# Kernel tuning notes

Measured on AMD Instinct MI355X. Metric: run time of the kernel, lower is better.

The kernel has to match this reference:

```python
import jax, jax.numpy as jnp
import numpy as np

N_NODES = 100000
N_EDGES = 1000000
F = 64
ALPHA = 0.1
BETA = 0.5


def setup_inputs() -> dict:
    key = jax.random.key(0)
    k1, k2, k3, k4, k5, k6 = jax.random.split(key, 6)
    features = jax.random.normal(k1, (N_NODES, F), dtype=jnp.float32)
    features0 = jax.random.normal(k2, (N_NODES, F), dtype=jnp.float32)
    edge_src = jax.random.randint(k3, (N_EDGES,), 0, N_NODES, dtype=jnp.int32)
    edge_dst = jax.random.randint(k4, (N_EDGES,), 0, N_NODES, dtype=jnp.int32)
    edge_vals = jax.random.uniform(k5, (N_EDGES,), dtype=jnp.float32)
    W = jax.random.normal(k6, (F, F), dtype=jnp.float32) * (1.0 / np.sqrt(F))
    return {"features": features, "features0": features0, "edge_src": edge_src,
            "edge_dst": edge_dst, "edge_vals": edge_vals, "W": W}


def reference(features, features0, edge_src, edge_dst, edge_vals, W):
    # hi = A @ features  (sparse propagation via edge-list segment sum)
    msgs = features[edge_src] * edge_vals[:, None]           # [E, F]
    hi = jax.ops.segment_sum(msgs, edge_dst, num_segments=N_NODES)  # [N, F]
    # variant=False branch of GCNII-style layer
    support = (1.0 - ALPHA) * hi + ALPHA * features0          # [N, F]
    r = support
    output = BETA * (support @ W) + (1.0 - BETA) * r          # [N, F]
    return jax.nn.relu(output)
```

## Files before the change

### kernel.cpp

```cpp
#include <hip/hip_runtime.h>

#define N_NODES 100000
#define N_EDGES 1000000
#define FDIM    64
#define TILES   6250
#define CAP     36

#define MM_BLOCKS  1024
#define EPB        2048
#define BIN_BLOCKS ((N_EDGES + EPB - 1) / EPB)

#define NPART 196
#define PCAP  9216

#define SCAN_BLOCKS 391

#define B_CNT   0u
#define B_GCUR  450560u
#define B_BKT   524288u
#define B_GBF   14924288u
#define B_NEED  27800000u

#define C_DEG    0u
#define C_OFFS   524288u
#define C_CURSOR 1048576u
#define C_BSUM   1572864u
#define C_BOFF   1703936u
#define C_BPACK  2097152u
#define C_GBF    6291456u

typedef short bf16x8 __attribute__((ext_vector_type(8)));
typedef float f32x4  __attribute__((ext_vector_type(4)));

__device__ __forceinline__ short f2bf(float f) {
    unsigned u = __float_as_uint(f);
    u += 0x7fff + ((u >> 16) & 1);
    return (short)(u >> 16);
}

__device__ __forceinline__ unsigned packrec(int s, float v) {
    unsigned q = (unsigned)__float2int_rn(v * 32768.0f);
    q = q > 32767u ? 32767u : q;
    return ((unsigned)s << 15) | q;
}

__global__ __launch_bounds__(256, 2) void k_fused(
        const float* __restrict__ feat, const float* __restrict__ f0,
        const float* __restrict__ W, unsigned short* __restrict__ gbf,
        float* __restrict__ out,
        const int* __restrict__ src, const int* __restrict__ dst,
        const float* __restrict__ val, int* __restrict__ cnt,
        unsigned* __restrict__ bkt, int* __restrict__ gcur, int binBlocks) {

    if ((int)blockIdx.x < binBlocks) {
        __shared__ int            hist[256];
        __shared__ int            excl[256];
        __shared__ int            curs[256];
        __shared__ int            gbas[256];
        __shared__ unsigned short slotpid[EPB];
        __shared__ uint2          rbuf[EPB];

        int t = threadIdx.x;
        hist[t] = 0;
        __syncthreads();

        int e0 = blockIdx.x * EPB + t * 8;
        unsigned recx[8]; int dd[8]; int pid[8]; bool vld[8];
        if (e0 + 8 <= N_EDGES) {
            int4   sa = *(const int4*)(src + e0);
            int4   sb = *(const int4*)(src + e0 + 4);
            int4   da = *(const int4*)(dst + e0);
            int4   db = *(const int4*)(dst + e0 + 4);
            float4 va = *(const float4*)(val + e0);
            float4 vb = *(const float4*)(val + e0 + 4);
            int   s8[8] = {sa.x, sa.y, sa.z, sa.w, sb.x, sb.y, sb.z, sb.w};
            int   d8[8] = {da.x, da.y, da.z, da.w, db.x, db.y, db.z, db.w};
            float v8[8] = {va.x, va.y, va.z, va.w, vb.x, vb.y, vb.z, vb.w};
#pragma unroll
            for (int j = 0; j < 8; ++j) {
                recx[j] = packrec(s8[j], v8[j]);
                dd[j]   = d8[j];
                pid[j]  = d8[j] >> 9;
                vld[j]  = true;
            }
        } else {
#pragma unroll
            for (int j = 0; j < 8; ++j) {
                vld[j] = (e0 + j) < N_EDGES;
                if (vld[j]) {
                    recx[j] = packrec(src[e0 + j], val[e0 + j]);
                    dd[j]   = dst[e0 + j];
                    pid[j]  = dd[j] >> 9;
                } else { recx[j] = 0; dd[j] = 0; pid[j] = 0; }
            }
        }
#pragma unroll
        for (int j = 0; j < 8; ++j)
            if (vld[j]) atomicAdd(&hist[pid[j]], 1);
        __syncthreads();

        int myv = hist[t];
        for (int off = 1; off < 256; off <<= 1) {
            int add = (t >= off) ? hist[t - off] : 0;
            __syncthreads();
            hist[t] += add;
            __syncthreads();
        }
        excl[t] = hist[t] - myv;
        curs[t] = excl[t];
        gbas[t] = (t < NPART && myv > 0) ? atomicAdd(&gcur[t], myv) : 0;
        __syncthreads();

#pragma unroll
        for (int j = 0; j < 8; ++j)
            if (vld[j]) {
                int pos = atomicAdd(&curs[pid[j]], 1);
                rbuf[pos]    = make_uint2(recx[j], (unsigned)dd[j]);
                slotpid[pos] = (unsigned short)pid[j];
            }
        __syncthreads();

        int total = hist[255];
        uint2* pbuf = (uint2*)bkt;
        for (int i = t; i < total; i += 256) {
            int p   = slotpid[i];
            int off = gbas[p] + (i - excl[p]);
            if (off < PCAP)
                pbuf[(size_t)p * PCAP + off] = rbuf[i];
        }
        return;
    }

    int lane = threadIdx.x & 63;
    int mmb  = blockIdx.x - binBlocks;
    int wid  = mmb * 4 + (threadIdx.x >> 6);
    int nw   = (gridDim.x - binBlocks) * 4;
    int n16  = lane & 15, q = lane >> 4;

    bf16x8 bf[2][4];
#pragma unroll
    for (int s = 0; s < 2; ++s)
#pragma unroll
        for (int t = 0; t < 4; ++t) {
            bf16x8 b;
#pragma unroll
            for (int j = 0; j < 8; ++j) {
                int k = 32 * s + 8 * q + j, n = 16 * t + n16;
                float m = 0.5f * W[k * FDIM + n] + (k == n ? 0.5f : 0.0f);
                b[j] = f2bf(m);
            }
            bf[s][t] = b;
        }

    for (int tid = wid; tid < 2 * TILES; tid += nw) {
        bool hpath = tid >= TILES;
        int  row0  = (hpath ? tid - TILES : tid) * 16;
        const float* x = (hpath ? f0 : feat) + (size_t)row0 * FDIM;

        bf16x8 af[2];
#pragma unroll
        for (int s = 0; s < 2; ++s) {
            const float* xp = x + (size_t)n16 * FDIM + 32 * s + 8 * q;
            float4 u0 = *(const float4*)xp;
            float4 u1 = *(const float4*)(xp + 4);
            bf16x8 a;
            a[0] = f2bf(u0.x); a[1] = f2bf(u0.y); a[2] = f2bf(u0.z); a[3] = f2bf(u0.w);
            a[4] = f2bf(u1.x); a[5] = f2bf(u1.y); a[6] = f2bf(u1.z); a[7] = f2bf(u1.w);
            af[s] = a;
        }

        f32x4 acc[4] = {{0,0,0,0},{0,0,0,0},{0,0,0,0},{0,0,0,0}};
#pragma unroll
        for (int s = 0; s < 2; ++s)
#pragma unroll
            for (int t = 0; t < 4; ++t)
                acc[t] = __builtin_amdgcn_mfma_f32_16x16x32_bf16(af[s], bf[s][t], acc[t], 0, 0, 0);

        if (!hpath) {
#pragma unroll
            for (int t = 0; t < 4; ++t)
#pragma unroll
                for (int r = 0; r < 4; ++r)
                    gbf[(size_t)(row0 + 4 * q + r) * FDIM + 16 * t + n16] =
                        (unsigned short)f2bf(acc[t][r]);
        } else {
#pragma unroll
            for (int t = 0; t < 4; ++t)
#pragma unroll
                for (int r = 0; r < 4; ++r)
                    out[(size_t)(row0 + 4 * q + r) * FDIM + 16 * t + n16] =
                        0.1f * acc[t][r];
        }
    }
}

__global__ __launch_bounds__(256) void k_p2(
        unsigned* __restrict__ bkt, int* __restrict__ cnt,
        const int* __restrict__ gcur) {
    __shared__ int      lcnt[512];
    __shared__ unsigned lbkt[512 * CAP];

    int p = blockIdx.x, t = threadIdx.x;
    int nE = gcur[p];
    if (nE > PCAP) nE = PCAP;

    for (int i = t; i < 512; i += 256) lcnt[i] = 0;
    __syncthreads();

    const uint2* pb = (const uint2*)bkt + (size_t)p * PCAP;
    for (int e = t; e < nE; e += 256) {
        uint2 r  = pb[e];
        int   ld = (int)r.y - (p << 9);
        int  pos = atomicAdd(&lcnt[ld], 1);
        if (pos < CAP) lbkt[ld * CAP + pos] = r.x;
    }
    __syncthreads();

    int nbase = p << 9;
    int nnode = N_NODES - nbase; if (nnode > 512) nnode = 512;
    unsigned* gb = bkt + (size_t)nbase * CAP;
    for (int i = t; i < nnode * CAP; i += 256) gb[i] = lbkt[i];
    for (int i = t; i < nnode;       i += 256) cnt[nbase + i] = lcnt[i];
}

__device__ __forceinline__ void gather_core(int node, int lane,
                                            const unsigned* base, int deg,
                                            const unsigned short* gbf,
                                            float* out) {
    int fl  = lane & 31;
    int sub = lane >> 5;

    float2 h = ((const float2*)(out + (size_t)node * FDIM))[fl];
    float accLo = 0.0f, accHi = 0.0f;

    for (int e0 = 0; e0 < deg; e0 += 16) {
        unsigned rsel[8];
        float    vsel[8];
#pragma unroll
        for (int j = 0; j < 8; ++j) {
            int i0 = e0 + 2 * j, i1 = i0 + 1;
            int c0 = i0 < deg ? i0 : deg - 1;
            int c1 = i1 < deg ? i1 : deg - 1;
            unsigned rA = base[c0];
            unsigned rB = base[c1];
            unsigned r  = sub ? rB : rA;
            bool ok = (sub ? i1 : i0) < deg;
            rsel[j] = r;
            vsel[j] = ok ? (float)(r & 0x7fffu) * (1.0f / 32768.0f) : 0.0f;
        }
        unsigned u[8];
#pragma unroll
        for (int j = 0; j < 8; ++j)
            u[j] = *(const unsigned*)(gbf + (size_t)(rsel[j] >> 15) * FDIM + 2 * fl);
#pragma unroll
        for (int j = 0; j < 8; ++j) {
            accLo = fmaf(vsel[j], __uint_as_float(u[j] << 16), accLo);
            accHi = fmaf(vsel[j], __uint_as_float(u[j] & 0xffff0000u), accHi);
        }
    }
    accLo += __shfl_xor(accLo, 32);
    accHi += __shfl_xor(accHi, 32);
    if (sub == 0) {
        float2 r2;
        r2.x = fmaxf(0.9f * accLo + h.x, 0.0f);
        r2.y = fmaxf(0.9f * accHi + h.y, 0.0f);
        ((float2*)(out + (size_t)node * FDIM))[fl] = r2;
    }
}

__global__ __launch_bounds__(256, 8) void k_gather_b(
        const int* __restrict__ cnt, const unsigned* __restrict__ bkt,
        const unsigned short* __restrict__ gbf, float* __restrict__ out) {
    int gid  = blockIdx.x * blockDim.x + threadIdx.x;
    int node = __builtin_amdgcn_readfirstlane(gid >> 6);
    int lane = threadIdx.x & 63;
    if (node >= N_NODES) return;
    int c = cnt[node];
    int deg = __builtin_amdgcn_readfirstlane(c < CAP ? c : CAP);
    gather_core(node, lane, bkt + (size_t)node * CAP, deg, gbf, out);
}

__global__ __launch_bounds__(256, 8) void k_gather_c(
        const int* __restrict__ offs, const unsigned* __restrict__ bpack,
        const unsigned short* __restrict__ gbf, float* __restrict__ out) {
    int gid  = blockIdx.x * blockDim.x + threadIdx.x;
    int node = __builtin_amdgcn_readfirstlane(gid >> 6);
    int lane = threadIdx.x & 63;
    if (node >= N_NODES) return;
    int beg = __builtin_amdgcn_readfirstlane(offs[node]);
    int end = __builtin_amdgcn_readfirstlane(
        (node == N_NODES - 1) ? N_EDGES : offs[node + 1]);
    gather_core(node, lane, bpack + beg, end - beg, gbf, out);
}

__global__ void k_hist(const int* __restrict__ dst, int* __restrict__ deg) {
    int e = blockIdx.x * blockDim.x + threadIdx.x;
    if (e < N_EDGES) atomicAdd(&deg[dst[e]], 1);
}

__global__ void k_scan1(const int* __restrict__ deg, int* __restrict__ bsum) {
    __shared__ int lds[256];
    int i = blockIdx.x * 256 + threadIdx.x;
    lds[threadIdx.x] = (i < N_NODES) ? deg[i] : 0;
    __syncthreads();
    for (int s = 128; s > 0; s >>= 1) {
        if (threadIdx.x < s) lds[threadIdx.x] += lds[threadIdx.x + s];
        __syncthreads();
    }
    if (threadIdx.x == 0) bsum[blockIdx.x] = lds[0];
}

__global__ void k_scan2(const int* __restrict__ bsum, int* __restrict__ boff) {
    __shared__ int lds[512];
    int t = threadIdx.x;
    int v = (t < SCAN_BLOCKS) ? bsum[t] : 0;
    lds[t] = v;
    __syncthreads();
    for (int off = 1; off < 512; off <<= 1) {
        int add = (t >= off) ? lds[t - off] : 0;
        __syncthreads();
        lds[t] += add;
        __syncthreads();
    }
    if (t < SCAN_BLOCKS) boff[t] = lds[t] - v;
}

__global__ void k_scan3(const int* __restrict__ deg, const int* __restrict__ boff,
                        int* __restrict__ offs, int* __restrict__ cursor) {
    __shared__ int lds[256];
    int t = threadIdx.x;
    int i = blockIdx.x * 256 + t;
    int v = (i < N_NODES) ? deg[i] : 0;
    lds[t] = v;
    __syncthreads();
    for (int off = 1; off < 256; off <<= 1) {
        int add = (t >= off) ? lds[t - off] : 0;
        __syncthreads();
        lds[t] += add;
        __syncthreads();
    }
    int excl = lds[t] - v + boff[blockIdx.x];
    if (i < N_NODES) { offs[i] = excl; cursor[i] = excl; }
}

__global__ void k_bin_c(const int* __restrict__ src, const int* __restrict__ dst,
                        const float* __restrict__ val, int* __restrict__ cursor,
                        unsigned* __restrict__ bpack) {
    int e = blockIdx.x * blockDim.x + threadIdx.x;
    if (e >= N_EDGES) return;
    int d = dst[e];
    int p = atomicAdd(&cursor[d], 1);
    bpack[p] = packrec(src[e], val[e]);
}

extern "C" void kernel_launch(void* const* d_in, const int* in_sizes, int n_in,
                              void* d_out, int out_size, void* d_ws, size_t ws_size,
                              hipStream_t stream) {
    const float* features  = (const float*)d_in[0];
    const float* features0 = (const float*)d_in[1];
    const int*   edge_src  = (const int*)d_in[2];
    const int*   edge_dst  = (const int*)d_in[3];
    const float* edge_vals = (const float*)d_in[4];
    const float* W         = (const float*)d_in[5];
    float*       out       = (float*)d_out;
    char*        ws        = (char*)d_ws;

    int eblocks = (N_EDGES + 255) / 256;
    int gblocks = (N_NODES + 3) / 4;

    if (ws_size >= B_NEED) {
        int*            cnt  = (int*)(ws + B_CNT);
        int*            gcur = (int*)(ws + B_GCUR);
        unsigned*       bkt  = (unsigned*)(ws + B_BKT);
        unsigned short* gbf  = (unsigned short*)(ws + B_GBF);

        hipMemsetAsync(gcur, 0, NPART * sizeof(int), stream);
        k_fused<<<BIN_BLOCKS + MM_BLOCKS, 256, 0, stream>>>(
            features, features0, W, gbf, out,
            edge_src, edge_dst, edge_vals, cnt, bkt, gcur, BIN_BLOCKS);
        k_p2<<<NPART, 256, 0, stream>>>(bkt, cnt, gcur);
        k_gather_b<<<gblocks, 256, 0, stream>>>(cnt, bkt, gbf, out);
    } else {
        int*            deg    = (int*)(ws + C_DEG);
        int*            offs   = (int*)(ws + C_OFFS);
        int*            cursor = (int*)(ws + C_CURSOR);
        int*            bsum   = (int*)(ws + C_BSUM);
        int*            boff   = (int*)(ws + C_BOFF);
        unsigned*       bpack  = (unsigned*)(ws + C_BPACK);
        unsigned short* gbf    = (unsigned short*)(ws + C_GBF);

        hipMemsetAsync(deg, 0, N_NODES * sizeof(int), stream);
        k_hist<<<eblocks, 256, 0, stream>>>(edge_dst, deg);
        k_scan1<<<SCAN_BLOCKS, 256, 0, stream>>>(deg, bsum);
        k_scan2<<<1, 512, 0, stream>>>(bsum, boff);
        k_scan3<<<SCAN_BLOCKS, 256, 0, stream>>>(deg, boff, offs, cursor);
        k_bin_c<<<eblocks, 256, 0, stream>>>(edge_src, edge_dst, edge_vals, cursor, bpack);
        k_fused<<<MM_BLOCKS, 256, 0, stream>>>(
            features, features0, W, gbf, out,
            edge_src, edge_dst, edge_vals, cursor, bpack, (int*)nullptr, 0);
        k_gather_c<<<gblocks, 256, 0, stream>>>(offs, bpack, gbf, out);
    }
}
```

Before: 172.9 us.

## Compact per-partition edge buckets and store the residual term as bf16

The partition pass now writes edges into a compact per-partition packed array with per-node offsets, built by an LDS scan at 512 threads. The old fixed-capacity padded slots were copied out whole, so less data is written and the gather reads contiguously. The residual term from the matmul is stored as bf16 in a separate buffer instead of fp32 in the output, which halves that read and write traffic. The binning histogram scan now uses wave shuffles instead of a barrier-heavy LDS loop. In exchange the workspace grows, the p2 kernel gains an extra scan, and bf16 rounding of the residual adds error.

```diff
diff --git a/kernel.cpp b/kernel.cpp
--- a/kernel.cpp
+++ b/kernel.cpp
@@ -5,6 +5,7 @@
 #define FDIM    64
 #define TILES   6250
 #define CAP     36
+#define LBS     37
 
 #define MM_BLOCKS  1024
 #define EPB        2048
@@ -16,18 +17,22 @@
 #define SCAN_BLOCKS 391
 
 #define B_CNT   0u
-#define B_GCUR  450560u
-#define B_BKT   524288u
-#define B_GBF   14924288u
-#define B_NEED  27800000u
+#define B_OFFS  409600u
+#define B_GCUR  819200u
+#define B_BKT   1048576u
+#define B_PK    15499264u
+#define B_PRE   22724608u
+#define B_GBF   35524608u
+#define B_NEED  48400000u
 
 #define C_DEG    0u
-#define C_OFFS   524288u
-#define C_CURSOR 1048576u
-#define C_BSUM   1572864u
-#define C_BOFF   1703936u
-#define C_BPACK  2097152u
-#define C_GBF    6291456u
+#define C_OFFS   409600u
+#define C_CURSOR 819200u
+#define C_BSUM   1228800u
+#define C_BOFF   1232896u
+#define C_BPACK  1236992u
+#define C_PRE    5242880u
+#define C_GBF    18042880u
 
 typedef short bf16x8 __attribute__((ext_vector_type(8)));
 typedef float f32x4  __attribute__((ext_vector_type(4)));
@@ -47,16 +52,17 @@
 __global__ __launch_bounds__(256, 2) void k_fused(
         const float* __restrict__ feat, const float* __restrict__ f0,
         const float* __restrict__ W, unsigned short* __restrict__ gbf,
-        float* __restrict__ out,
+        unsigned short* __restrict__ preBf,
         const int* __restrict__ src, const int* __restrict__ dst,
-        const float* __restrict__ val, int* __restrict__ cnt,
+        const float* __restrict__ val,
         unsigned* __restrict__ bkt, int* __restrict__ gcur, int binBlocks) {
 
     if ((int)blockIdx.x < binBlocks) {
-        __shared__ int            hist[256];
         __shared__ int            excl[256];
         __shared__ int            curs[256];
         __shared__ int            gbas[256];
+        __shared__ int            hist[256];
+        __shared__ int            wsum[4];
         __shared__ unsigned short slotpid[EPB];
         __shared__ uint2          rbuf[EPB];
 
@@ -99,15 +105,25 @@
             if (vld[j]) atomicAdd(&hist[pid[j]], 1);
         __syncthreads();
 
-        int myv = hist[t];
-        for (int off = 1; off < 256; off <<= 1) {
-            int add = (t >= off) ? hist[t - off] : 0;
-            __syncthreads();
-            hist[t] += add;
-            __syncthreads();
-        }
-        excl[t] = hist[t] - myv;
-        curs[t] = excl[t];
+        int myv  = hist[t];
+        int lanev = myv;
+#pragma unroll
+        for (int off = 1; off < 64; off <<= 1) {
+            int nv = __shfl_up(lanev, off, 64);
+            if ((t & 63) >= off) lanev += nv;
+        }
+        if ((t & 63) == 63) wsum[t >> 6] = lanev;
+        __syncthreads();
+        int prev = 0, total = 0;
+#pragma unroll
+        for (int w = 0; w < 4; ++w) {
+            int s = wsum[w];
+            prev  += (w < (t >> 6)) ? s : 0;
+            total += s;
+        }
+        int ex = lanev + prev - myv;
+        excl[t] = ex;
+        curs[t] = ex;
         gbas[t] = (t < NPART && myv > 0) ? atomicAdd(&gcur[t], myv) : 0;
         __syncthreads();
 
@@ -120,7 +136,6 @@
             }
         __syncthreads();
 
-        int total = hist[255];
         uint2* pbuf = (uint2*)bkt;
         for (int i = t; i < total; i += 256) {
             int p   = slotpid[i];
@@ -188,49 +203,66 @@
             for (int t = 0; t < 4; ++t)
 #pragma unroll
                 for (int r = 0; r < 4; ++r)
-                    out[(size_t)(row0 + 4 * q + r) * FDIM + 16 * t + n16] =
-                        0.1f * acc[t][r];
-        }
-    }
-}
-
-__global__ __launch_bounds__(256) void k_p2(
-        unsigned* __restrict__ bkt, int* __restrict__ cnt,
+                    preBf[(size_t)(row0 + 4 * q + r) * FDIM + 16 * t + n16] =
+                        (unsigned short)f2bf(0.1f * acc[t][r]);
+        }
+    }
+}
+
+__global__ __launch_bounds__(512) void k_p2(
+        const unsigned* __restrict__ bkt, unsigned* __restrict__ pk,
+        int* __restrict__ offs, int* __restrict__ cnt,
         const int* __restrict__ gcur) {
     __shared__ int      lcnt[512];
-    __shared__ unsigned lbkt[512 * CAP];
+    __shared__ int      loff[512];
+    __shared__ unsigned lbkt[512 * LBS];
 
     int p = blockIdx.x, t = threadIdx.x;
     int nE = gcur[p];
     if (nE > PCAP) nE = PCAP;
 
-    for (int i = t; i < 512; i += 256) lcnt[i] = 0;
+    lcnt[t] = 0;
     __syncthreads();
 
     const uint2* pb = (const uint2*)bkt + (size_t)p * PCAP;
-    for (int e = t; e < nE; e += 256) {
+    for (int e = t; e < nE; e += 512) {
         uint2 r  = pb[e];
         int   ld = (int)r.y - (p << 9);
         int  pos = atomicAdd(&lcnt[ld], 1);
-        if (pos < CAP) lbkt[ld * CAP + pos] = r.x;
-    }
-    __syncthreads();
-
-    int nbase = p << 9;
-    int nnode = N_NODES - nbase; if (nnode > 512) nnode = 512;
-    unsigned* gb = bkt + (size_t)nbase * CAP;
-    for (int i = t; i < nnode * CAP; i += 256) gb[i] = lbkt[i];
-    for (int i = t; i < nnode;       i += 256) cnt[nbase + i] = lcnt[i];
+        if (pos < CAP) lbkt[ld * LBS + pos] = r.x;
+    }
+    __syncthreads();
+
+    int c = lcnt[t]; if (c > CAP) c = CAP;
+    loff[t] = c;
+    __syncthreads();
+    for (int off = 1; off < 512; off <<= 1) {
+        int add = (t >= off) ? loff[t - off] : 0;
+        __syncthreads();
+        loff[t] += add;
+        __syncthreads();
+    }
+    int beg = loff[t] - c;
+
+    int node = (p << 9) + t;
+    if (node < N_NODES) {
+        offs[node] = p * PCAP + beg;
+        cnt[node]  = c;
+    }
+
+    unsigned* dp = pk + (size_t)p * PCAP + beg;
+    for (int i = 0; i < c; ++i) dp[i] = lbkt[t * LBS + i];
 }
 
 __device__ __forceinline__ void gather_core(int node, int lane,
                                             const unsigned* base, int deg,
                                             const unsigned short* gbf,
+                                            const unsigned short* preBf,
                                             float* out) {
     int fl  = lane & 31;
     int sub = lane >> 5;
 
-    float2 h = ((const float2*)(out + (size_t)node * FDIM))[fl];
+    unsigned hp = ((const unsigned*)(preBf + (size_t)node * FDIM))[fl];
     float accLo = 0.0f, accHi = 0.0f;
 
     for (int e0 = 0; e0 < deg; e0 += 16) {
@@ -262,27 +294,30 @@
     accHi += __shfl_xor(accHi, 32);
     if (sub == 0) {
         float2 r2;
-        r2.x = fmaxf(0.9f * accLo + h.x, 0.0f);
-        r2.y = fmaxf(0.9f * accHi + h.y, 0.0f);
+        r2.x = fmaxf(0.9f * accLo + __uint_as_float(hp << 16), 0.0f);
+        r2.y = fmaxf(0.9f * accHi + __uint_as_float(hp & 0xffff0000u), 0.0f);
         ((float2*)(out + (size_t)node * FDIM))[fl] = r2;
     }
 }
 
 __global__ __launch_bounds__(256, 8) void k_gather_b(
-        const int* __restrict__ cnt, const unsigned* __restrict__ bkt,
-        const unsigned short* __restrict__ gbf, float* __restrict__ out) {
+        const int* __restrict__ cnt, const int* __restrict__ offs,
+        const unsigned* __restrict__ pk,
+        const unsigned short* __restrict__ gbf,
+        const unsigned short* __restrict__ preBf, float* __restrict__ out) {
     int gid  = blockIdx.x * blockDim.x + threadIdx.x;
     int node = __builtin_amdgcn_readfirstlane(gid >> 6);
     int lane = threadIdx.x & 63;
     if (node >= N_NODES) return;
-    int c = cnt[node];
-    int deg = __builtin_amdgcn_readfirstlane(c < CAP ? c : CAP);
-    gather_core(node, lane, bkt + (size_t)node * CAP, deg, gbf, out);
+    int deg = __builtin_amdgcn_readfirstlane(cnt[node]);
+    int beg = __builtin_amdgcn_readfirstlane(offs[node]);
+    gather_core(node, lane, pk + beg, deg, gbf, preBf, out);
 }
 
 __global__ __launch_bounds__(256, 8) void k_gather_c(
         const int* __restrict__ offs, const unsigned* __restrict__ bpack,
-        const unsigned short* __restrict__ gbf, float* __restrict__ out) {
+        const unsigned short* __restrict__ gbf,
+        const unsigned short* __restrict__ preBf, float* __restrict__ out) {
     int gid  = blockIdx.x * blockDim.x + threadIdx.x;
     int node = __builtin_amdgcn_readfirstlane(gid >> 6);
     int lane = threadIdx.x & 63;
@@ -290,7 +325,7 @@
     int beg = __builtin_amdgcn_readfirstlane(offs[node]);
     int end = __builtin_amdgcn_readfirstlane(
         (node == N_NODES - 1) ? N_EDGES : offs[node + 1]);
-    gather_core(node, lane, bpack + beg, end - beg, gbf, out);
+    gather_core(node, lane, bpack + beg, end - beg, gbf, preBf, out);
 }
 
 __global__ void k_hist(const int* __restrict__ dst, int* __restrict__ deg) {
@@ -369,17 +404,20 @@
     int gblocks = (N_NODES + 3) / 4;
 
     if (ws_size >= B_NEED) {
-        int*            cnt  = (int*)(ws + B_CNT);
-        int*            gcur = (int*)(ws + B_GCUR);
-        unsigned*       bkt  = (unsigned*)(ws + B_BKT);
-        unsigned short* gbf  = (unsigned short*)(ws + B_GBF);
+        int*            cnt   = (int*)(ws + B_CNT);
+        int*            offs  = (int*)(ws + B_OFFS);
+        int*            gcur  = (int*)(ws + B_GCUR);
+        unsigned*       bkt   = (unsigned*)(ws + B_BKT);
+        unsigned*       pk    = (unsigned*)(ws + B_PK);
+        unsigned short* preBf = (unsigned short*)(ws + B_PRE);
+        unsigned short* gbf   = (unsigned short*)(ws + B_GBF);
 
         hipMemsetAsync(gcur, 0, NPART * sizeof(int), stream);
         k_fused<<<BIN_BLOCKS + MM_BLOCKS, 256, 0, stream>>>(
-            features, features0, W, gbf, out,
-            edge_src, edge_dst, edge_vals, cnt, bkt, gcur, BIN_BLOCKS);
-        k_p2<<<NPART, 256, 0, stream>>>(bkt, cnt, gcur);
-        k_gather_b<<<gblocks, 256, 0, stream>>>(cnt, bkt, gbf, out);
+            features, features0, W, gbf, preBf,
+            edge_src, edge_dst, edge_vals, bkt, gcur, BIN_BLOCKS);
+        k_p2<<<NPART, 512, 0, stream>>>(bkt, pk, offs, cnt, gcur);
+        k_gather_b<<<gblocks, 256, 0, stream>>>(cnt, offs, pk, gbf, preBf, out);
     } else {
         int*            deg    = (int*)(ws + C_DEG);
         int*            offs   = (int*)(ws + C_OFFS);
@@ -387,6 +425,7 @@
         int*            bsum   = (int*)(ws + C_BSUM);
         int*            boff   = (int*)(ws + C_BOFF);
         unsigned*       bpack  = (unsigned*)(ws + C_BPACK);
+        unsigned short* preBf  = (unsigned short*)(ws + C_PRE);
         unsigned short* gbf    = (unsigned short*)(ws + C_GBF);
 
         hipMemsetAsync(deg, 0, N_NODES * sizeof(int), stream);
@@ -396,8 +435,8 @@
         k_scan3<<<SCAN_BLOCKS, 256, 0, stream>>>(deg, boff, offs, cursor);
         k_bin_c<<<eblocks, 256, 0, stream>>>(edge_src, edge_dst, edge_vals, cursor, bpack);
         k_fused<<<MM_BLOCKS, 256, 0, stream>>>(
-            features, features0, W, gbf, out,
-            edge_src, edge_dst, edge_vals, cursor, bpack, (int*)nullptr, 0);
-        k_gather_c<<<gblocks, 256, 0, stream>>>(offs, bpack, gbf, out);
-    }
-}
+            features, features0, W, gbf, preBf,
+            edge_src, edge_dst, edge_vals, (unsigned*)nullptr, (int*)nullptr, 0);
+        k_gather_c<<<gblocks, 256, 0, stream>>>(offs, bpack, gbf, preBf, out);
+    }
+}
```

After: 165.9 us. 1.04x faster.
